# Performance work log

Measured on AMD Instinct MI355X. Metric: run time of the kernel, lower is better.

The kernel has to match this reference:

```python
import jax, jax.numpy as jnp
import numpy as np

VALUE_RANGE = 16
D_MODEL = 1024
NUM_TILES = 8
NUM_FREQS = 6
BATCH = 65536
TEMPERATURE = 0.5


def _fourier(x):
    # x: (B,) -> (B, 2*NUM_FREQS); freqs = 2**[0..F)
    freqs = 2.0 ** jnp.arange(NUM_FREQS, dtype=jnp.float32)
    ang = x[:, None] * (2.0 * np.pi / VALUE_RANGE) * freqs[None, :]
    return jnp.concatenate([jnp.sin(ang), jnp.cos(ang)], axis=-1)


def _layernorm(x, g, b, eps=1e-5):
    m = jnp.mean(x, axis=-1, keepdims=True)
    v = jnp.var(x, axis=-1, keepdims=True)
    return (x - m) * jax.lax.rsqrt(v + eps) * g + b


def _gelu(x):
    return jax.nn.gelu(x, approximate=False)  # torch nn.GELU() default is exact erf


def setup_inputs() -> dict:
    key = jax.random.key(0)
    ks = jax.random.split(key, 16)
    d, T, F4 = D_MODEL, NUM_TILES, 4 * NUM_FREQS
    s = lambda i, shape, scale: (jax.random.normal(ks[i], shape, jnp.float32) * scale)
    return {
        "a": jax.random.uniform(ks[0], (BATCH,), jnp.float32, 0.0, float(VALUE_RANGE)),
        "b": jax.random.uniform(ks[1], (BATCH,), jnp.float32, 0.0, float(VALUE_RANGE)),
        "W_in": s(2, (F4, d), 0.05), "b_in": jnp.zeros((d,), jnp.float32),
        "ln_g": jnp.ones((d,), jnp.float32), "ln_b": jnp.zeros((d,), jnp.float32),
        "Wr1_sum": s(3, (d, d), 0.03), "br1_sum": jnp.zeros((d,), jnp.float32),
        "Wr2_sum": s(4, (d, T), 0.03), "br2_sum": jnp.zeros((T,), jnp.float32),
        "Wr1_diff": s(5, (d, d), 0.03), "br1_diff": jnp.zeros((d,), jnp.float32),
        "Wr2_diff": s(6, (d, T), 0.03), "br2_diff": jnp.zeros((T,), jnp.float32),
        "We1": s(7, (T, d, 2 * d), 0.03), "be1": jnp.zeros((T, 2 * d), jnp.float32),
        "We2": s(8, (T, 2 * d, d), 0.02), "be2": jnp.zeros((T, d), jnp.float32),
        "w_sum": s(9, (d,), 0.03), "bs": jnp.zeros((), jnp.float32),
        "w_diff": s(10, (d,), 0.03), "bd": jnp.zeros((), jnp.float32),
    }


def reference(a, b, W_in, b_in, ln_g, ln_b,
              Wr1_sum, br1_sum, Wr2_sum, br2_sum,
              Wr1_diff, br1_diff, Wr2_diff, br2_diff,
              We1, be1, We2, be2, w_sum, bs, w_diff, bd):
    # Shared encoder
    x = jnp.concatenate([_fourier(a), _fourier(b)], axis=-1)      # (B, 4F)
    x = _gelu(_layernorm(x @ W_in + b_in, ln_g, ln_b))            # (B, d)
    # Top-1 routing (temperature scaling does not change argmax, kept for fidelity)
    sum_logits = (_gelu(x @ Wr1_sum + br1_sum) @ Wr2_sum + br2_sum) / TEMPERATURE
    diff_logits = (_gelu(x @ Wr1_diff + br1_diff) @ Wr2_diff + br2_diff) / TEMPERATURE
    sum_tile = jnp.argmax(sum_logits, axis=-1)                    # (B,)
    diff_tile = jnp.argmax(diff_logits, axis=-1)                  # (B,)
    # Expert dispatch: loop over small fixed num_tiles, mask-combine per token.
    sum_hidden = jnp.zeros_like(x)
    diff_hidden = jnp.zeros_like(x)
    for t in range(We1.shape[0]):
        y = _gelu(x @ We1[t] + be1[t]) @ We2[t] + be2[t]          # (B, d)
        sum_hidden = sum_hidden + jnp.where((sum_tile == t)[:, None], y, 0.0)
        diff_hidden = diff_hidden + jnp.where((diff_tile == t)[:, None], y, 0.0)
    sum_pred = sum_hidden @ w_sum + bs                            # (B,)
    diff_pred = diff_hidden @ w_diff + bd                         # (B,)
    return (sum_pred, diff_pred)
```

## Files before the change

### kernel.cpp

```cpp
#include <hip/hip_runtime.h>
#include <math.h>


#define BT 65536
#define D 1024
#define NT 8
#define DH 2048
#define RCAP 8192
#define DELTA 0.010f
#define XJCAP 768

typedef _Float16 f16;
typedef _Float16 f16x8 __attribute__((ext_vector_type(8)));
typedef _Float16 f16x4 __attribute__((ext_vector_type(4)));
typedef float f32x16 __attribute__((ext_vector_type(16)));

__device__ __forceinline__ float gelu_f(float v) {
    return 0.5f * v * (1.0f + erff(v * 0.70710678118654752440f));
}

__device__ __forceinline__ float gelu_fast(float x) {
    float ax = fabsf(x) * 0.70710678118654752440f;
    float t = __builtin_amdgcn_rcpf(1.0f + 0.3275911f * ax);
    float p = t * (0.254829592f + t * (-0.284496736f + t * (1.421413741f +
              t * (-1.453152027f + t * 1.061405429f))));
    float er = 1.0f - p * __expf(-ax * ax);
    er = copysignf(er, x);
    return 0.5f * x * (1.0f + er);
}

__device__ __forceinline__ void gload16(const void* g, void* l) {
    __builtin_amdgcn_global_load_lds(
        (const __attribute__((address_space(1))) void*)g,
        (__attribute__((address_space(3))) void*)l, 16, 0, 0);
}

__global__ __launch_bounds__(256) void k_prev(
    const float* __restrict__ We2, const float* __restrict__ w_sum,
    const float* __restrict__ w_diff, const float* __restrict__ be2,
    const float* __restrict__ bs, const float* __restrict__ bd,
    float* __restrict__ v_sum, float* __restrict__ v_diff,
    float* __restrict__ c_sum, float* __restrict__ c_diff)
{
    int bid = blockIdx.x;
    if (bid < 4096) {
        int row  = bid * 4 + (threadIdx.x >> 6);
        int lane = threadIdx.x & 63;
        const float* r = We2 + (size_t)row * D;
        float s1 = 0.f, s2 = 0.f;
        #pragma unroll
        for (int i = 0; i < 4; i++) {
            int o4 = (lane + 64 * i) * 4;
            float4 w = *(const float4*)(r + o4);
            float4 u = *(const float4*)(w_sum + o4);
            float4 v = *(const float4*)(w_diff + o4);
            s1 += w.x*u.x + w.y*u.y + w.z*u.z + w.w*u.w;
            s2 += w.x*v.x + w.y*v.y + w.z*v.z + w.w*v.w;
        }
        #pragma unroll
        for (int m = 32; m >= 1; m >>= 1) {
            s1 += __shfl_xor(s1, m, 64);
// ... 36 lines not shown
    for (int i = 0; i < 16; i++) {
        int idx = tid + 256 * i;
        int nn = idx >> 6, kk = idx & 63;
        dst[(size_t)nn * D + kk] = (f16)tile[kk][nn];
    }
}

__global__ __launch_bounds__(256) void k_cvtR(
    const float* __restrict__ Wr1s, const float* __restrict__ Wr1d,
    f16* __restrict__ Wr1Tf)
{
    __shared__ float tile[64][65];
    int b = blockIdx.x;
    int z = b >> 8, rem = b & 255;
    int kt = rem >> 4, nt2 = rem & 15;
    int tid = threadIdx.x;
    const float* W = z ? Wr1d : Wr1s;
    const float* src = W + (size_t)(kt * 64) * 1024 + nt2 * 64;
    #pragma unroll
    for (int i = 0; i < 16; i++) {
        int idx = tid + 256 * i;
        int kk = idx >> 6, nn = idx & 63;
        tile[kk][nn] = src[(size_t)kk * 1024 + nn];
    }
    __syncthreads();
    f16* dst = Wr1Tf + (size_t)(z * 1024 + nt2 * 64) * 1024 + kt * 64;
    #pragma unroll
    for (int i = 0; i < 16; i++) {
        int idx = tid + 256 * i;
        int nn = idx >> 6, kk = idx & 63;
        dst[(size_t)nn * 1024 + kk] = (f16)tile[kk][nn];
    }
}

__global__ __launch_bounds__(256) void k_fuse(
    const float* __restrict__ br1s, const float* __restrict__ br1d,
    const float* __restrict__ Wr2s, const float* __restrict__ Wr2d,
    float* __restrict__ br1f, float* __restrict__ w2f)
{
    int tid = threadIdx.x;
    for (int n = tid; n < 2048; n += 256) {
        br1f[n] = (n < 1024) ? br1s[n] : br1d[n - 1024];
        const float* src = (n < 1024) ? (Wr2s + (size_t)n * 8)
                                      : (Wr2d + (size_t)(n - 1024) * 8);
        #pragma unroll
        for (int o = 0; o < 8; o++) w2f[(size_t)n * 8 + o] = src[o];
    }
}

__global__ __launch_bounds__(256) void k_enc(
    const float* __restrict__ a, const float* __restrict__ b,
    const float* __restrict__ W_in, const float* __restrict__ b_in,
    const float* __restrict__ ln_g, const float* __restrict__ ln_b,
    float* __restrict__ x, f16* __restrict__ xh, int tok0)
{
    __shared__ float x0[64][24];
    __shared__ float red[8];
    int tid = threadIdx.x;
    float4 Wc[24];
    #pragma unroll
    for (int f = 0; f < 24; f++) Wc[f] = *(const float4*)(W_in + f * D + tid * 4);
    float4 bi = *(const float4*)(b_in + tid * 4);
    float4 gg = *(const float4*)(ln_g + tid * 4);
    float4 bb = *(const float4*)(ln_b + tid * 4);
    int base = tok0 + blockIdx.x * 64;

    for (int idx = tid; idx < 64 * 12; idx += 256) {
        int t = idx / 12, q = idx - t * 12;
        int fr = q % 6;
        float in = (q < 6) ? a[base + t] : b[base + t];
        float ang = (in * 0.39269908169872414f) * (float)(1 << fr);
        int off = (q < 6) ? 0 : 12;
        x0[t][off + fr]     = sinf(ang);
        x0[t][off + 6 + fr] = cosf(ang);
    }
    __syncthreads();

    int lane = tid & 63, wid = tid >> 6;
    for (int t = 0; t < 64; t++) {
        float4 p = bi;
        #pragma unroll
        for (int f = 0; f < 24; f++) {
            float xv = x0[t][f];
            p.x += xv * Wc[f].x; p.y += xv * Wc[f].y;
            p.z += xv * Wc[f].z; p.w += xv * Wc[f].w;
        }
        float s1 = p.x + p.y + p.z + p.w;
        float s2 = p.x*p.x + p.y*p.y + p.z*p.z + p.w*p.w;
        #pragma unroll
        for (int m = 32; m >= 1; m >>= 1) {
            s1 += __shfl_xor(s1, m, 64);
            s2 += __shfl_xor(s2, m, 64);
        }
        if (lane == 0) { red[wid] = s1; red[4 + wid] = s2; }
        __syncthreads();
        float mean = (red[0] + red[1] + red[2] + red[3]) * (1.f / 1024.f);
        float ms   = (red[4] + red[5] + red[6] + red[7]) * (1.f / 1024.f);
        float inv  = 1.f / sqrtf(ms - mean * mean + 1e-5f);
        float4 o;
        o.x = gelu_f((p.x - mean) * inv * gg.x + bb.x);
        o.y = gelu_f((p.y - mean) * inv * gg.y + bb.y);
        o.z = gelu_f((p.z - mean) * inv * gg.z + bb.z);
        o.w = gelu_f((p.w - mean) * inv * gg.w + bb.w);
        size_t row = (size_t)(blockIdx.x * 64 + t);
        *(float4*)(x + row * D + tid * 4) = o;
        f16x4 h; h[0] = (f16)o.x; h[1] = (f16)o.y; h[2] = (f16)o.z; h[3] = (f16)o.w;
        *(f16x4*)(xh + row * D + tid * 4) = h;
        __syncthreads();
    }
}

__global__ __launch_bounds__(256, 3) void k_rtrm(
    const f16* __restrict__ xh, const f16* __restrict__ Wr1Tf,
    const float* __restrict__ br1f, const float* __restrict__ w2f,
    float* __restrict__ part)
{
    __shared__ char smem[40960] __attribute__((aligned(16)));
    int bid = blockIdx.x;
    int ntile = bid & 7;
    int ttile = bid >> 3;
    int tid = threadIdx.x;
    int lane = tid & 63, wid = tid >> 6;
    int hi = lane >> 5, l31 = lane & 31;
    int sg = tid >> 3, sc = tid & 7;

    const char* xb = (const char*)xh + (size_t)(ttile * 64) * 2048;
    const char* wb = (const char*)Wr1Tf + (size_t)(ntile * 256) * 2048;
    size_t goff = (size_t)sg * 2048 + (size_t)((sc * 16) ^ ((sg & 7) << 4));

    int axor = (l31 & 7) << 4;
    int kx[4];
    #pragma unroll
    for (int ks = 0; ks < 4; ks++) kx[ks] = (ks * 32 + hi * 16) ^ axor;
    int arow[2], brow[2];
    #pragma unroll
    for (int mi = 0; mi < 2; mi++) arow[mi] = (wid * 64 + mi * 32 + l31) * 128;
    #pragma unroll
    for (int ni = 0; ni < 2; ni++) brow[ni] = 32768 + (ni * 32 + l31) * 128;

    f32x16 acc[2][2];
    #pragma unroll
    for (int mi = 0; mi < 2; mi++)
        #pragma unroll
        for (int ni = 0; ni < 2; ni++) acc[mi][ni] = (f32x16)(0.0f);

    for (int k0 = 0; k0 < 1024; k0 += 64) {
        __syncthreads();
        #pragma unroll
        for (int i = 0; i < 8; i++)
            gload16(wb + (size_t)i * 32 * 2048 + k0 * 2 + goff,
                    smem + i * 4096 + wid * 1024);
        #pragma unroll
        for (int i = 0; i < 2; i++)
            gload16(xb + (size_t)i * 32 * 2048 + k0 * 2 + goff,
                    smem + 32768 + i * 4096 + wid * 1024);
        __syncthreads();
        #pragma unroll
        for (int ks = 0; ks < 4; ks++) {
// ... 4 lines not shown
            acc[0][0] = __builtin_amdgcn_mfma_f32_32x32x16_f16(a0, b0, acc[0][0], 0, 0, 0);
            acc[0][1] = __builtin_amdgcn_mfma_f32_32x32x16_f16(a0, b1, acc[0][1], 0, 0, 0);
            acc[1][0] = __builtin_amdgcn_mfma_f32_32x32x16_f16(a1, b0, acc[1][0], 0, 0, 0);
            acc[1][1] = __builtin_amdgcn_mfma_f32_32x32x16_f16(a1, b1, acc[1][1], 0, 0, 0);
        }
    }

    float lp[2][8] = {};
    #pragma unroll
    for (int mi = 0; mi < 2; mi++) {
        #pragma unroll
        for (int r = 0; r < 16; r++) {
            int nl = wid * 64 + mi * 32 + (r & 3) + 8 * (r >> 2) + 4 * hi;
            int gn = ntile * 256 + nl;
            float b1 = br1f[gn];
            float4 wa = *(const float4*)(w2f + (size_t)gn * 8);
            float4 wc = *(const float4*)(w2f + (size_t)gn * 8 + 4);
            float h0 = gelu_fast(acc[mi][0][r] + b1);
            float h1 = gelu_fast(acc[mi][1][r] + b1);
            lp[0][0] += h0*wa.x; lp[0][1] += h0*wa.y;
            lp[0][2] += h0*wa.z; lp[0][3] += h0*wa.w;
            lp[0][4] += h0*wc.x; lp[0][5] += h0*wc.y;
            lp[0][6] += h0*wc.z; lp[0][7] += h0*wc.w;
            lp[1][0] += h1*wa.x; lp[1][1] += h1*wa.y;
            lp[1][2] += h1*wa.z; lp[1][3] += h1*wa.w;
            lp[1][4] += h1*wc.x; lp[1][5] += h1*wc.y;
            lp[1][6] += h1*wc.z; lp[1][7] += h1*wc.w;
        }
    }
    #pragma unroll
    for (int ni = 0; ni < 2; ni++)
        #pragma unroll
        for (int o = 0; o < 8; o++)
            lp[ni][o] += __shfl_xor(lp[ni][o], 32, 64);
    __syncthreads();
    float* redf = (float*)smem;
    if (hi == 0) {
        #pragma unroll
        for (int ni = 0; ni < 2; ni++)
            #pragma unroll
            for (int o = 0; o < 8; o++)
                redf[(wid * 64 + ni * 32 + l31) * 8 + o] = lp[ni][o];
    }
    __syncthreads();
    for (int idx = tid; idx < 512; idx += 256) {
        int tok = idx >> 3, o = idx & 7;
        float s = ((redf[(0 * 64 + tok) * 8 + o]  + redf[(1 * 64 + tok) * 8 + o])
                 +  redf[(2 * 64 + tok) * 8 + o]) + redf[(3 * 64 + tok) * 8 + o];
        part[((size_t)(ttile * 64 + tok) * 8 + ntile) * 8 + o] = s;
    }
}

__device__ __forceinline__ void emit_tasks(int tok, int ts, int td,
                                           int* tasks, int* cnts, int tstr)
{
    if (ts == td) {
        int s = atomicAdd(&cnts[ts], 1);
        tasks[ts * tstr + s] = tok | (3 << 17);
    } else {
        int s1 = atomicAdd(&cnts[ts], 1);
        tasks[ts * tstr + s1] = tok | (1 << 17);
        int s2 = atomicAdd(&cnts[td], 1);
        tasks[td * tstr + s2] = tok | (2 << 17);
    }
}

__global__ __launch_bounds__(256) void k_amx2(
    const float* __restrict__ part, const float* __restrict__ b2s,
    const float* __restrict__ b2d, int* __restrict__ tasks,
    int* __restrict__ ctrl, int* __restrict__ redoS, int* __restrict__ redoD,
    int tstr)
{
    int i = blockIdx.x * 256 + threadIdx.x;
    const float* p = part + (size_t)i * 64;
    float Ls[8], Ld[8];
    #pragma unroll
    for (int o = 0; o < 8; o++) { Ls[o] = b2s[o]; Ld[o] = b2d[o]; }
    #pragma unroll
    for (int nt = 0; nt < 4; nt++)
        #pragma unroll
        for (int o = 0; o < 8; o++) Ls[o] += p[nt * 8 + o];
    #pragma unroll
    for (int nt = 4; nt < 8; nt++)
        #pragma unroll
        for (int o = 0; o < 8; o++) Ld[o] += p[nt * 8 + o];

    int as = 0; float m1s = Ls[0];
    #pragma unroll
    for (int o = 1; o < 8; o++) if (Ls[o] > m1s) { m1s = Ls[o]; as = o; }
    float m2s = -1e30f;
    #pragma unroll
    for (int o = 0; o < 8; o++) if (o != as && Ls[o] > m2s) m2s = Ls[o];
    int ad = 0; float m1d = Ld[0];
    #pragma unroll
    for (int o = 1; o < 8; o++) if (Ld[o] > m1d) { m1d = Ld[o]; ad = o; }
    float m2d = -1e30f;
    #pragma unroll
    for (int o = 0; o < 8; o++) if (o != ad && Ld[o] > m2d) m2d = Ld[o];

    bool sM = (m1s - m2s) < DELTA;
    bool dM = (m1d - m2d) < DELTA;
    if (!sM && !dM) { emit_tasks(i, as, ad, tasks, ctrl, tstr); return; }
    int posS = -1, posD = -1;
    if (sM) { posS = atomicAdd(&ctrl[8], 1); if (posS >= RCAP) { sM = false; posS = -1; } }
    if (dM) { posD = atomicAdd(&ctrl[9], 1); if (posD >= RCAP) { dM = false; posD = -1; } }
    if (!sM && !dM) { emit_tasks(i, as, ad, tasks, ctrl, tstr); return; }
    if (sM) redoS[posS] = i | (ad << 17) | ((dM ? 1 : 0) << 20);
    if (dM) redoD[posD] = i | (as << 17) | ((sM ? 1 : 0) << 20);
}

__global__ __launch_bounds__(256) void k_redo(
    const float* __restrict__ x,
    const float* __restrict__ Wr1s, const float* __restrict__ br1s,
    const float* __restrict__ Wr2s,
    const float* __restrict__ Wr1d, const float* __restrict__ br1d,
    const float* __restrict__ Wr2d,
    const int* __restrict__ redoS, const int* __restrict__ redoD,
    const int* __restrict__ ctrl,
    float* __restrict__ rlogpS, float* __restrict__ rlogpD)
{
    int nt = blockIdx.y, z = blockIdx.z;
    int rcnt = min(ctrl[8 + z], RCAP);
    const float* Wr1 = z ? Wr1d : Wr1s;
    const float* br1 = z ? br1d : br1s;
    const float* Wr2 = z ? Wr2d : Wr2s;
    const int* list = z ? redoD : redoS;
    float* rlogp = z ? rlogpD : rlogpS;
    __shared__ float As[64][72];
    __shared__ float Bs[64][132];
    __shared__ int tokR[64];
    int tid = threadIdx.x;
    int tr = tid >> 5, tc = tid & 31;

    for (int mc = blockIdx.x; mc * 64 < rcnt; mc += gridDim.x) {
        __syncthreads();
        if (tid < 64) tokR[tid] = list[min(mc * 64 + tid, rcnt - 1)] & 0xFFFF;
        __syncthreads();
        float acc[8][4] = {};
        const float* wb = Wr1 + nt * 128;
        for (int k0 = 0; k0 < D; k0 += 64) {
            __syncthreads();
            {
                int row = tid >> 2, q = tid & 3;
                const float* xr = x + (size_t)tokR[row] * D + k0;
                #pragma unroll
                for (int i = 0; i < 4; i++) {
                    int f4i = q + 4 * i;
                    float4 v = *(const float4*)(xr + f4i * 4);
                    int k = f4i * 4;
                    As[k][row] = v.x; As[k+1][row] = v.y;
                    As[k+2][row] = v.z; As[k+3][row] = v.w;
                }
            }
            {
                #pragma unroll
                for (int i = 0; i < 8; i++) {
                    int idx = tid + 256 * i;
                    int k = idx >> 5, nq = idx & 31;
                    float4 v = *(const float4*)(wb + (size_t)(k0 + k) * D + nq * 4);
                    *(float4*)&Bs[k][nq * 4] = v;
                }
            }
            __syncthreads();
            #pragma unroll 4
            for (int kk = 0; kk < 64; kk++) {
                float4 a0 = *(const float4*)&As[kk][tr * 8];
                float4 a1 = *(const float4*)&As[kk][tr * 8 + 4];
                float4 bv = *(const float4*)&Bs[kk][tc * 4];
                float ar[8] = {a0.x,a0.y,a0.z,a0.w,a1.x,a1.y,a1.z,a1.w};
                #pragma unroll
                for (int i = 0; i < 8; i++) {
                    acc[i][0] += ar[i] * bv.x;
                    acc[i][1] += ar[i] * bv.y;
                    acc[i][2] += ar[i] * bv.z;
                    acc[i][3] += ar[i] * bv.w;
                }
            }
        }
        float lp[8][8] = {};
        #pragma unroll
        for (int j = 0; j < 4; j++) {
            int col = nt * 128 + tc * 4 + j;
            float b1 = br1[col];
            float w2[8];
            #pragma unroll
            for (int o = 0; o < 8; o++) w2[o] = Wr2[col * 8 + o];
            #pragma unroll
            for (int i = 0; i < 8; i++) {
                float h = gelu_f(acc[i][j] + b1);
                #pragma unroll
                for (int o = 0; o < 8; o++) lp[i][o] += h * w2[o];
            }
        }
        #pragma unroll
        for (int m = 16; m >= 1; m >>= 1) {
            #pragma unroll
            for (int i = 0; i < 8; i++)
                #pragma unroll
                for (int o = 0; o < 8; o++)
                    lp[i][o] += __shfl_xor(lp[i][o], m, 64);
        }
        if (tc == 0) {
            #pragma unroll
            for (int i = 0; i < 8; i++) {
                int slot = mc * 64 + tr * 8 + i;
                if (slot < rcnt) {
                    float* p = rlogp + (size_t)slot * 64 + nt * 8;
                    #pragma unroll
                    for (int o = 0; o < 8; o++) p[o] = lp[i][o];
                }
            }
        }
    }
}

__global__ __launch_bounds__(256) void k_amx3d(
    const float* __restrict__ rlogpD, const int* __restrict__ redoD,
    const float* __restrict__ b2d, int* __restrict__ tasks,
    int* __restrict__ ctrl, int* __restrict__ adx, int tstr)
{
    int rcnt = min(ctrl[9], RCAP);
    for (int s = blockIdx.x * 256 + threadIdx.x; s < rcnt; s += gridDim.x * 256) {
        int entry = redoD[s];
        int tok = entry & 0xFFFF;
        float L[8] = {};
        for (int nt = 0; nt < 8; nt++) {
            const float* p = rlogpD + (size_t)s * 64 + nt * 8;
            #pragma unroll
            for (int o = 0; o < 8; o++) L[o] += p[o];
        }
        #pragma unroll
        for (int o = 0; o < 8; o++) L[o] += b2d[o];
        int td = 0; float bv = L[0];
        #pragma unroll
        for (int o = 1; o < 8; o++) if (L[o] > bv) { bv = L[o]; td = o; }
        adx[tok] = td;
        if (!((entry >> 20) & 1))
            emit_tasks(tok, (entry >> 17) & 7, td, tasks, ctrl, tstr);
    }
}

__global__ __launch_bounds__(256) void k_amx3s(
    const float* __restrict__ rlogpS, const int* __restrict__ redoS,
    const float* __restrict__ b2s, int* __restrict__ tasks,
    int* __restrict__ ctrl, const int* __restrict__ adx, int tstr)
{
    int rcnt = min(ctrl[8], RCAP);
    for (int s = blockIdx.x * 256 + threadIdx.x; s < rcnt; s += gridDim.x * 256) {
        int entry = redoS[s];
        int tok = entry & 0xFFFF;
        float L[8] = {};
        for (int nt = 0; nt < 8; nt++) {
            const float* p = rlogpS + (size_t)s * 64 + nt * 8;
            #pragma unroll
            for (int o = 0; o < 8; o++) L[o] += p[o];
        }
        #pragma unroll
        for (int o = 0; o < 8; o++) L[o] += b2s[o];
        int ts = 0; float bv = L[0];
        #pragma unroll
        for (int o = 1; o < 8; o++) if (L[o] > bv) { bv = L[o]; ts = o; }
        int td = ((entry >> 20) & 1) ? adx[tok] : ((entry >> 17) & 7);
        emit_tasks(tok, ts, td, tasks, ctrl, tstr);
    }
}

__global__ void k_sched(const int* __restrict__ ctrl, int* __restrict__ xjob)
{
    __shared__ int seg[17];
    __shared__ int Jt[2];
    int tid = threadIdx.x;
    if (tid == 0) {
        int o = 0;
        for (int e = 0; e < 8; e++) {
            int nt2 = (ctrl[e] + 127) >> 7;
            seg[e * 2]     = o; o += nt2;
            seg[e * 2 + 1] = o; o += nt2;
        }
        seg[16] = o;
        Jt[0] = o; Jt[1] = (o + 7) >> 3;
    }
    __syncthreads();
    int J = Jt[0], target = Jt[1];
    for (int g = tid; g < J; g += blockDim.x) {
        int s = 0;
        while (s < 15 && seg[s + 1] <= g) s++;
        int e = s >> 1, ch = s & 1, rt = g - seg[s];
        int x = g / target; if (x > 7) x = 7;
        int pos = g - x * target;
        xjob[x * XJCAP + pos] = e | (ch << 3) | (rt << 4);
    }
    if (tid < 8) {
        int c = J - tid * target;
        if (c < 0) c = 0;
        if (c > target) c = target;
        xjob[8 * XJCAP + tid] = c;
    }
}

__global__ __launch_bounds__(256) void k_expm(
    const f16* __restrict__ xh, const f16* __restrict__ We1T,
    const float* __restrict__ be1, const float* __restrict__ v_sum,
    const float* __restrict__ v_diff, const float* __restrict__ c_sum,
    const float* __restrict__ c_diff, const int* __restrict__ tasks,
    const int* __restrict__ counts, const int* __restrict__ xjob,
    float* __restrict__ ppS, float* __restrict__ ppD, int qn)
{
    int xcd  = blockIdx.x & 7;
    int slot = blockIdx.x >> 3;
    int nj = xjob[8 * XJCAP + xcd];
    int tstr = 2 * qn;

    __shared__ char smem[49152] __attribute__((aligned(16)));
    __shared__ int tokL[128];
    __shared__ int flgL[128];
    __shared__ float redS[2][128];
    __shared__ float redD[2][128];

    int tid = threadIdx.x;
    int lane = tid & 63;
    int wid  = tid >> 6;
    int wr = wid >> 1, wc = wid & 1;
    int hi = lane >> 5, l31 = lane & 31;
    int sg = tid >> 3, sc = tid & 7;
    int stoff = sg * 128 + ((sc * 16) ^ ((sg & 7) << 4));

    const char* xh_b = (const char*)xh;

    int axor = (l31 & 7) << 4;
    int kx[4];
    #pragma unroll
    for (int ks = 0; ks < 4; ks++) kx[ks] = (ks * 32 + hi * 16) ^ axor;
    int arow[2], nrow[4];
    #pragma unroll
    for (int mi = 0; mi < 2; mi++) arow[mi] = (wr * 64 + mi * 32 + l31) * 128;
    #pragma unroll
    for (int ni = 0; ni < 4; ni++) nrow[ni] = 16384 + (wc * 128 + ni * 32 + l31) * 128;

    for (int j = slot; j < nj; j += 256) {
        int jv = xjob[xcd * XJCAP + j];
        int e  = jv & 7;
        int ch = (jv >> 3) & 1;
        int rt = jv >> 4;
        int cnt = counts[e];
        int r0 = rt * 128;
        const char* we1t_e = (const char*)(We1T + (size_t)e * DH * D);
        size_t bs_off = (size_t)sg * (D * 2) + sc * 16;

        __syncthreads();
        if (tid < 128) {
            int idx = r0 + tid;
            int tv = tasks[e * tstr + min(idx, cnt - 1)];
            tokL[tid] = tv & 0xFFFF;
            flgL[tid] = (idx < cnt) ? ((tv >> 17) & 3) : 0;
        }
        __syncthreads();
        size_t asrc_off[4];
        #pragma unroll
        for (int i = 0; i < 4; i++)
            asrc_off[i] = (size_t)tokL[i * 32 + sg] * (D * 2) + sc * 16;

        float ss[2][16] = {}, sd[2][16] = {};

        for (int n0 = ch * 1024; n0 < ch * 1024 + 1024; n0 += 256) {
            f32x16 acc[2][4];
            #pragma unroll
            for (int mi = 0; mi < 2; mi++)
                #pragma unroll
                for (int ni = 0; ni < 4; ni++)
                    acc[mi][ni] = (f32x16)(0.0f);

            const char* bsrc0 = we1t_e + (size_t)n0 * (D * 2) + bs_off;

            for (int k0 = 0; k0 < D; k0 += 64) {
                __syncthreads();
                #pragma unroll
                for (int i = 0; i < 4; i++) {
                    int4 v = *(const int4*)(xh_b + asrc_off[i] + k0 * 2);
                    *(int4*)(smem + i * 4096 + stoff) = v;
                }
                #pragma unroll
                for (int i = 0; i < 8; i++) {
                    int4 v = *(const int4*)(bsrc0 + (size_t)i * 32 * (D * 2) + k0 * 2);
                    *(int4*)(smem + 16384 + i * 4096 + stoff) = v;
                }
                __syncthreads();
                #pragma unroll
                for (int ks = 0; ks < 4; ks++) {
                    f16x8 a0 = *(const f16x8*)(smem + arow[0] + kx[ks]);
                    f16x8 a1 = *(const f16x8*)(smem + arow[1] + kx[ks]);
                    #pragma unroll
                    for (int ni = 0; ni < 4; ni++) {
                        f16x8 bf = *(const f16x8*)(smem + nrow[ni] + kx[ks]);
                        acc[0][ni] = __builtin_amdgcn_mfma_f32_32x32x16_f16(a0, bf, acc[0][ni], 0, 0, 0);
                        acc[1][ni] = __builtin_amdgcn_mfma_f32_32x32x16_f16(a1, bf, acc[1][ni], 0, 0, 0);
                    }
                }
            }
            #pragma unroll
            for (int ni = 0; ni < 4; ni++) {
                int col = n0 + wc * 128 + ni * 32 + l31;
                float b1 = be1[e * DH + col];
                float vs = v_sum[(size_t)e * DH + col];
                float vd = v_diff[(size_t)e * DH + col];
                #pragma unroll
                for (int mi = 0; mi < 2; mi++) {
                    #pragma unroll
                    for (int r = 0; r < 16; r++) {
                        float h = gelu_fast(acc[mi][ni][r] + b1);
                        ss[mi][r] += h * vs;
                        sd[mi][r] += h * vd;
                    }
                }
            }
        }

        #pragma unroll
        for (int m = 16; m >= 1; m >>= 1) {
            #pragma unroll
            for (int mi = 0; mi < 2; mi++)
                #pragma unroll
                for (int r = 0; r < 16; r++) {
                    ss[mi][r] += __shfl_xor(ss[mi][r], m, 64);
                    sd[mi][r] += __shfl_xor(sd[mi][r], m, 64);
                }
        }
        if (l31 == 0) {
            #pragma unroll
            for (int mi = 0; mi < 2; mi++)
                #pragma unroll
                for (int r = 0; r < 16; r++) {
                    int row = wr * 64 + mi * 32 + (r & 3) + 8 * (r >> 2) + 4 * hi;
                    redS[wc][row] = ss[mi][r];
                    redD[wc][row] = sd[mi][r];
                }
        }
        __syncthreads();
        if (tid < 128) {
            int idx = r0 + tid;
            if (idx < cnt) {
                int fl = flgL[tid];
                int tok = tokL[tid];
                float s = redS[0][tid] + redS[1][tid];
                float d = redD[0][tid] + redD[1][tid];
                if (ch == 0) { s += c_sum[e]; d += c_diff[e]; }
                if (fl & 1) ppS[ch * qn + tok] = s;
                if (fl & 2) ppD[ch * qn + tok] = d;
            }
        }
    }
}

__global__ __launch_bounds__(256) void k_fin(
    const float* __restrict__ ppS, const float* __restrict__ ppD,
    float* __restrict__ out, int tok0, int qn)
{
    int i = blockIdx.x * 256 + threadIdx.x;
    out[tok0 + i]      = ppS[i] + ppS[qn + i];
    out[BT + tok0 + i] = ppD[i] + ppD[qn + i];
}

extern "C" void kernel_launch(void* const* d_in, const int* in_sizes, int n_in,
                              void* d_out, int out_size, void* d_ws, size_t ws_size,
                              hipStream_t stream)
{
    const float* a      = (const float*)d_in[0];
    const float* b      = (const float*)d_in[1];
    const float* W_in   = (const float*)d_in[2];
    const float* b_in   = (const float*)d_in[3];
    const float* ln_g   = (const float*)d_in[4];
    const float* ln_b   = (const float*)d_in[5];
    const float* Wr1s   = (const float*)d_in[6];
    const float* br1s   = (const float*)d_in[7];
    const float* Wr2s   = (const float*)d_in[8];
    const float* br2s   = (const float*)d_in[9];
    const float* Wr1d   = (const float*)d_in[10];
    const float* br1d   = (const float*)d_in[11];
    const float* Wr2d   = (const float*)d_in[12];
    const float* br2d   = (const float*)d_in[13];
    const float* We1    = (const float*)d_in[14];
    const float* be1    = (const float*)d_in[15];
    const float* We2    = (const float*)d_in[16];
    const float* be2    = (const float*)d_in[17];
    const float* w_sum  = (const float*)d_in[18];
    const float* bs     = (const float*)d_in[19];
    const float* w_diff = (const float*)d_in[20];
    const float* bd     = (const float*)d_in[21];
    float* out = (float*)d_out;

    auto plan = [&](size_t qn) -> size_t {
        size_t o = 0;
        auto al = [&](size_t bytes) { o = (o + bytes + 255) & ~(size_t)255; };
        al((size_t)NT * DH * 4); al((size_t)NT * DH * 4); al(64); al(64);
        al(qn * D * 4); al(qn * D * 2); al(qn * 64 * 4);
        al((size_t)RCAP * 64 * 4); al((size_t)RCAP * 64 * 4);
        al((size_t)RCAP * 4); al((size_t)RCAP * 4); al(qn * 4);
        al((size_t)NT * 2 * qn * 4);
        al(64); al((size_t)(8 * XJCAP + 8) * 4);
        al(2 * qn * 4); al(2 * qn * 4);
        al((size_t)NT * DH * D * 2); al((size_t)2048 * 1024 * 2);
        al(2048 * 4); al(2048 * 8 * 4);
        return o;
    };
    int qn = 65536;
    while (qn > 16384 && plan((size_t)qn) > ws_size) qn >>= 1;
    if (plan((size_t)qn) > ws_size) {
        hipMemsetAsync(d_out, 0, (size_t)out_size * 4, stream);
        return;
    }
    int npass = BT / qn;
    int tstr = 2 * qn;

    char* w = (char*)d_ws;
    size_t off = 0;
    auto alloc = [&](size_t bytes) -> char* {
        char* p = w + off;
        off = (off + bytes + 255) & ~(size_t)255;
        return p;
    };
    float* v_sum   = (float*)alloc((size_t)NT * DH * 4);
    float* v_diff  = (float*)alloc((size_t)NT * DH * 4);
    float* c_sum   = (float*)alloc(64);
    float* c_diff  = (float*)alloc(64);
    float* x       = (float*)alloc((size_t)qn * D * 4);
    f16*   xh      = (f16*)alloc((size_t)qn * D * 2);
    float* part    = (float*)alloc((size_t)qn * 64 * 4);
    float* rlogpS  = (float*)alloc((size_t)RCAP * 64 * 4);
    float* rlogpD  = (float*)alloc((size_t)RCAP * 64 * 4);
    int*   redoS   = (int*)alloc((size_t)RCAP * 4);
    int*   redoD   = (int*)alloc((size_t)RCAP * 4);
    int*   adx     = (int*)alloc((size_t)qn * 4);
    int*   tasks   = (int*)alloc((size_t)NT * 2 * qn * 4);
    int*   ctrl    = (int*)alloc(64);
    int*   xjob    = (int*)alloc((size_t)(8 * XJCAP + 8) * 4);
    float* ppS     = (float*)alloc((size_t)2 * qn * 4);
    float* ppD     = (float*)alloc((size_t)2 * qn * 4);
    f16*   We1T    = (f16*)alloc((size_t)NT * DH * D * 2);
    f16*   Wr1Tf   = (f16*)alloc((size_t)2048 * 1024 * 2);
    float* br1f    = (float*)alloc((size_t)2048 * 4);
    float* w2f     = (float*)alloc((size_t)2048 * 8 * 4);

    k_cvt <<<dim3(4096), dim3(256), 0, stream>>>(We1, We1T);
    k_cvtR<<<dim3(512),  dim3(256), 0, stream>>>(Wr1s, Wr1d, Wr1Tf);
    k_fuse<<<dim3(1),    dim3(256), 0, stream>>>(br1s, br1d, Wr2s, Wr2d, br1f, w2f);
    k_prev<<<dim3(4097), dim3(256), 0, stream>>>(We2, w_sum, w_diff, be2, bs, bd,
                                                 v_sum, v_diff, c_sum, c_diff);
    for (int q = 0; q < npass; q++) {
        int tok0 = q * qn;
        k_enc<<<dim3(qn / 64), dim3(256), 0, stream>>>(a, b, W_in, b_in, ln_g, ln_b, x, xh, tok0);
        k_rtrm<<<dim3(qn / 64 * 8), dim3(256), 0, stream>>>(xh, Wr1Tf, br1f, w2f, part);
        hipMemsetAsync(ctrl, 0, 64, stream);
        k_amx2<<<dim3(qn / 256), dim3(256), 0, stream>>>(part, br2s, br2d, tasks, ctrl,
                                                         redoS, redoD, tstr);
        k_redo<<<dim3(32, 8, 2), dim3(256), 0, stream>>>(x, Wr1s, br1s, Wr2s, Wr1d, br1d, Wr2d,
                                                         redoS, redoD, ctrl, rlogpS, rlogpD);
        k_amx3d<<<dim3(16), dim3(256), 0, stream>>>(rlogpD, redoD, br2d, tasks, ctrl, adx, tstr);
        k_amx3s<<<dim3(16), dim3(256), 0, stream>>>(rlogpS, redoS, br2s, tasks, ctrl, adx, tstr);
        k_sched<<<dim3(1), dim3(256), 0, stream>>>(ctrl, xjob);
        k_expm<<<dim3(2048), dim3(256), 0, stream>>>(xh, We1T, be1, v_sum, v_diff,
                                                     c_sum, c_diff, tasks, ctrl, xjob,
                                                     ppS, ppD, qn);
        k_fin<<<dim3(qn / 256), dim3(256), 0, stream>>>(ppS, ppD, out, tok0, qn);
    }
}
```

Baseline: 2.474 ms.

## Drop fp32 activation buffer, recompute encoder in redo, restructure expert GEMM loop

The encoder no longer writes a 256MB fp32 copy of the activations. The redo kernel now recomputes the encoder for each ambiguous token in small groups and computes the full router row per block, instead of tiling over a stored fp32 buffer. The expert GEMM kernel flattens its N/K loops into a single loop with register-prefetched B tiles and sets launch bounds to 2 blocks per SM. The multi-pass planning is removed, so buffers are sized for a single full-batch pass and the task stride is halved. This saves encoder write bandwidth at the cost of some redundant encoder compute and a fixed workspace requirement.

```diff
diff --git a/kernel.cpp b/kernel.cpp
--- a/kernel.cpp
+++ b/kernel.cpp
@@ -3,10 +3,13 @@
 
 
 #define BT 65536
+#define QN 65536
+#define TSTR QN
 #define D 1024
 #define NT 8
 #define DH 2048
 #define RCAP 8192
+#define RTOK 8
 #define DELTA 0.010f
 #define XJCAP 768
 
@@ -149,7 +152,7 @@
     const float* __restrict__ a, const float* __restrict__ b,
     const float* __restrict__ W_in, const float* __restrict__ b_in,
     const float* __restrict__ ln_g, const float* __restrict__ ln_b,
-    float* __restrict__ x, f16* __restrict__ xh, int tok0)
+    f16* __restrict__ xh)
 {
     __shared__ float x0[64][24];
     __shared__ float red[8];
@@ -160,7 +163,7 @@
     float4 bi = *(const float4*)(b_in + tid * 4);
     float4 gg = *(const float4*)(ln_g + tid * 4);
     float4 bb = *(const float4*)(ln_b + tid * 4);
-    int base = tok0 + blockIdx.x * 64;
+    int base = blockIdx.x * 64;
 
     for (int idx = tid; idx < 64 * 12; idx += 256) {
         int t = idx / 12, q = idx - t * 12;
@@ -200,7 +203,6 @@
         o.z = gelu_f((p.z - mean) * inv * gg.z + bb.z);
         o.w = gelu_f((p.w - mean) * inv * gg.w + bb.w);
         size_t row = (size_t)(blockIdx.x * 64 + t);
-        *(float4*)(x + row * D + tid * 4) = o;
         f16x4 h; h[0] = (f16)o.x; h[1] = (f16)o.y; h[2] = (f16)o.z; h[3] = (f16)o.w;
         *(f16x4*)(xh + row * D + tid * 4) = h;
         __syncthreads();
@@ -311,24 +313,23 @@
 }
 
 __device__ __forceinline__ void emit_tasks(int tok, int ts, int td,
-                                           int* tasks, int* cnts, int tstr)
+                                           int* tasks, int* cnts)
 {
     if (ts == td) {
         int s = atomicAdd(&cnts[ts], 1);
-        tasks[ts * tstr + s] = tok | (3 << 17);
+        tasks[ts * TSTR + s] = tok | (3 << 17);
     } else {
         int s1 = atomicAdd(&cnts[ts], 1);
-        tasks[ts * tstr + s1] = tok | (1 << 17);
+        tasks[ts * TSTR + s1] = tok | (1 << 17);
         int s2 = atomicAdd(&cnts[td], 1);
-        tasks[td * tstr + s2] = tok | (2 << 17);
+        tasks[td * TSTR + s2] = tok | (2 << 17);
     }
 }
 
 __global__ __launch_bounds__(256) void k_amx2(
     const float* __restrict__ part, const float* __restrict__ b2s,
     const float* __restrict__ b2d, int* __restrict__ tasks,
-    int* __restrict__ ctrl, int* __restrict__ redoS, int* __restrict__ redoD,
-    int tstr)
+    int* __restrict__ ctrl, int* __restrict__ redoS, int* __restrict__ redoD)
 {
     int i = blockIdx.x * 256 + threadIdx.x;
     const float* p = part + (size_t)i * 64;
@@ -359,17 +360,19 @@
 
     bool sM = (m1s - m2s) < DELTA;
     bool dM = (m1d - m2d) < DELTA;
-    if (!sM && !dM) { emit_tasks(i, as, ad, tasks, ctrl, tstr); return; }
+    if (!sM && !dM) { emit_tasks(i, as, ad, tasks, ctrl); return; }
     int posS = -1, posD = -1;
     if (sM) { posS = atomicAdd(&ctrl[8], 1); if (posS >= RCAP) { sM = false; posS = -1; } }
     if (dM) { posD = atomicAdd(&ctrl[9], 1); if (posD >= RCAP) { dM = false; posD = -1; } }
-    if (!sM && !dM) { emit_tasks(i, as, ad, tasks, ctrl, tstr); return; }
+    if (!sM && !dM) { emit_tasks(i, as, ad, tasks, ctrl); return; }
     if (sM) redoS[posS] = i | (ad << 17) | ((dM ? 1 : 0) << 20);
     if (dM) redoD[posD] = i | (as << 17) | ((sM ? 1 : 0) << 20);
 }
 
 __global__ __launch_bounds__(256) void k_redo(
-    const float* __restrict__ x,
+    const float* __restrict__ a, const float* __restrict__ b,
+    const float* __restrict__ W_in, const float* __restrict__ b_in,
+    const float* __restrict__ ln_g, const float* __restrict__ ln_b,
     const float* __restrict__ Wr1s, const float* __restrict__ br1s,
     const float* __restrict__ Wr2s,
     const float* __restrict__ Wr1d, const float* __restrict__ br1d,
@@ -378,97 +381,128 @@
     const int* __restrict__ ctrl,
     float* __restrict__ rlogpS, float* __restrict__ rlogpD)
 {
-    int nt = blockIdx.y, z = blockIdx.z;
+    int z = blockIdx.y;
     int rcnt = min(ctrl[8 + z], RCAP);
+    int s0 = blockIdx.x * RTOK;
+    if (s0 >= rcnt) return;
+    const int* list = z ? redoD : redoS;
     const float* Wr1 = z ? Wr1d : Wr1s;
-    const float* br1 = z ? br1d : br1s;
+    const float* br1v = z ? br1d : br1s;
     const float* Wr2 = z ? Wr2d : Wr2s;
-    const int* list = z ? redoD : redoS;
-    float* rlogp = z ? rlogpD : rlogpS;
-    __shared__ float As[64][72];
-    __shared__ float Bs[64][132];
-    __shared__ int tokR[64];
+
+    __shared__ float xl[RTOK][1024];
+    __shared__ float x0[RTOK][24];
+    __shared__ float wred[4][RTOK][2];
+    __shared__ float lred[4][RTOK][8];
+    __shared__ int tokR[RTOK];
     int tid = threadIdx.x;
-    int tr = tid >> 5, tc = tid & 31;
-
-    for (int mc = blockIdx.x; mc * 64 < rcnt; mc += gridDim.x) {
+    int lane = tid & 63, wid = tid >> 6;
+
+    if (tid < RTOK) tokR[tid] = list[min(s0 + tid, rcnt - 1)] & 0xFFFF;
+    __syncthreads();
+
+    if (tid < RTOK * 12) {
+        int t = tid / 12, q = tid - t * 12;
+        int fr = q % 6;
+        int tok = tokR[t];
+        float in = (q < 6) ? a[tok] : b[tok];
+        float ang = (in * 0.39269908169872414f) * (float)(1 << fr);
+        int off = (q < 6) ? 0 : 12;
+        x0[t][off + fr]     = sinf(ang);
+        x0[t][off + 6 + fr] = cosf(ang);
+    }
+    __syncthreads();
+
+    {
+        float4 Wc[24];
+        #pragma unroll
+        for (int f = 0; f < 24; f++) Wc[f] = *(const float4*)(W_in + f * D + tid * 4);
+        float4 bi = *(const float4*)(b_in + tid * 4);
+        float4 gg = *(const float4*)(ln_g + tid * 4);
+        float4 bb = *(const float4*)(ln_b + tid * 4);
+        float p[RTOK][4];
+        #pragma unroll
+        for (int r = 0; r < RTOK; r++) {
+            float4 pv = bi;
+            #pragma unroll
+            for (int f = 0; f < 24; f++) {
+                float xv = x0[r][f];
+                pv.x += xv * Wc[f].x; pv.y += xv * Wc[f].y;
+                pv.z += xv * Wc[f].z; pv.w += xv * Wc[f].w;
+            }
+            p[r][0] = pv.x; p[r][1] = pv.y; p[r][2] = pv.z; p[r][3] = pv.w;
+            float s1 = pv.x + pv.y + pv.z + pv.w;
+            float s2 = pv.x*pv.x + pv.y*pv.y + pv.z*pv.z + pv.w*pv.w;
+            #pragma unroll
+            for (int m = 32; m >= 1; m >>= 1) {
+                s1 += __shfl_xor(s1, m, 64);
+                s2 += __shfl_xor(s2, m, 64);
+            }
+            if (lane == 0) { wred[wid][r][0] = s1; wred[wid][r][1] = s2; }
+        }
         __syncthreads();
-        if (tid < 64) tokR[tid] = list[min(mc * 64 + tid, rcnt - 1)] & 0xFFFF;
-        __syncthreads();
-        float acc[8][4] = {};
-        const float* wb = Wr1 + nt * 128;
-        for (int k0 = 0; k0 < D; k0 += 64) {
-            __syncthreads();
-            {
-                int row = tid >> 2, q = tid & 3;
-                const float* xr = x + (size_t)tokR[row] * D + k0;
-                #pragma unroll
-                for (int i = 0; i < 4; i++) {
-                    int f4i = q + 4 * i;
-                    float4 v = *(const float4*)(xr + f4i * 4);
-                    int k = f4i * 4;
-                    As[k][row] = v.x; As[k+1][row] = v.y;
-                    As[k+2][row] = v.z; As[k+3][row] = v.w;
-                }
-            }
-            {
-                #pragma unroll
-                for (int i = 0; i < 8; i++) {
-                    int idx = tid + 256 * i;
-                    int k = idx >> 5, nq = idx & 31;
-                    float4 v = *(const float4*)(wb + (size_t)(k0 + k) * D + nq * 4);
-                    *(float4*)&Bs[k][nq * 4] = v;
-                }
-            }
-            __syncthreads();
-            #pragma unroll 4
-            for (int kk = 0; kk < 64; kk++) {
-                float4 a0 = *(const float4*)&As[kk][tr * 8];
-                float4 a1 = *(const float4*)&As[kk][tr * 8 + 4];
-                float4 bv = *(const float4*)&Bs[kk][tc * 4];
-                float ar[8] = {a0.x,a0.y,a0.z,a0.w,a1.x,a1.y,a1.z,a1.w};
-                #pragma unroll
-                for (int i = 0; i < 8; i++) {
-                    acc[i][0] += ar[i] * bv.x;
-                    acc[i][1] += ar[i] * bv.y;
-                    acc[i][2] += ar[i] * bv.z;
-                    acc[i][3] += ar[i] * bv.w;
-                }
-            }
-        }
-        float lp[8][8] = {};
-        #pragma unroll
-        for (int j = 0; j < 4; j++) {
-            int col = nt * 128 + tc * 4 + j;
-            float b1 = br1[col];
-            float w2[8];
-            #pragma unroll
-            for (int o = 0; o < 8; o++) w2[o] = Wr2[col * 8 + o];
-            #pragma unroll
-            for (int i = 0; i < 8; i++) {
-                float h = gelu_f(acc[i][j] + b1);
-                #pragma unroll
-                for (int o = 0; o < 8; o++) lp[i][o] += h * w2[o];
-            }
-        }
-        #pragma unroll
-        for (int m = 16; m >= 1; m >>= 1) {
-            #pragma unroll
-            for (int i = 0; i < 8; i++)
-                #pragma unroll
-                for (int o = 0; o < 8; o++)
-                    lp[i][o] += __shfl_xor(lp[i][o], m, 64);
-        }
-        if (tc == 0) {
-            #pragma unroll
-            for (int i = 0; i < 8; i++) {
-                int slot = mc * 64 + tr * 8 + i;
-                if (slot < rcnt) {
-                    float* p = rlogp + (size_t)slot * 64 + nt * 8;
-                    #pragma unroll
-                    for (int o = 0; o < 8; o++) p[o] = lp[i][o];
-                }
-            }
+        #pragma unroll
+        for (int r = 0; r < RTOK; r++) {
+            float mean = (wred[0][r][0] + wred[1][r][0] + wred[2][r][0] + wred[3][r][0]) * (1.f / 1024.f);
+            float ms   = (wred[0][r][1] + wred[1][r][1] + wred[2][r][1] + wred[3][r][1]) * (1.f / 1024.f);
+            float inv  = 1.f / sqrtf(ms - mean * mean + 1e-5f);
+            float gv[4] = {gg.x, gg.y, gg.z, gg.w};
+            float bv[4] = {bb.x, bb.y, bb.z, bb.w};
+            #pragma unroll
+            for (int jj = 0; jj < 4; jj++)
+                xl[r][tid * 4 + jj] = gelu_f((p[r][jj] - mean) * inv * gv[jj] + bv[jj]);
+        }
+    }
+    __syncthreads();
+
+    int c0 = tid * 4;
+    float hacc[RTOK][4] = {};
+    #pragma unroll 4
+    for (int k = 0; k < 1024; k++) {
+        float4 wv = *(const float4*)(Wr1 + (size_t)k * 1024 + c0);
+        #pragma unroll
+        for (int r = 0; r < RTOK; r++) {
+            float xv = xl[r][k];
+            hacc[r][0] += xv * wv.x; hacc[r][1] += xv * wv.y;
+            hacc[r][2] += xv * wv.z; hacc[r][3] += xv * wv.w;
+        }
+    }
+    float L[RTOK][8] = {};
+    #pragma unroll
+    for (int jj = 0; jj < 4; jj++) {
+        int col = c0 + jj;
+        float b1 = br1v[col];
+        float4 wa = *(const float4*)(Wr2 + (size_t)col * 8);
+        float4 wc = *(const float4*)(Wr2 + (size_t)col * 8 + 4);
+        #pragma unroll
+        for (int r = 0; r < RTOK; r++) {
+            float h = gelu_f(hacc[r][jj] + b1);
+            L[r][0] += h*wa.x; L[r][1] += h*wa.y; L[r][2] += h*wa.z; L[r][3] += h*wa.w;
+            L[r][4] += h*wc.x; L[r][5] += h*wc.y; L[r][6] += h*wc.z; L[r][7] += h*wc.w;
+        }
+    }
+    #pragma unroll
+    for (int m = 32; m >= 1; m >>= 1)
+        #pragma unroll
+        for (int r = 0; r < RTOK; r++)
+            #pragma unroll
+            for (int o = 0; o < 8; o++)
+                L[r][o] += __shfl_xor(L[r][o], m, 64);
+    if (lane == 0) {
+        #pragma unroll
+        for (int r = 0; r < RTOK; r++)
+            #pragma unroll
+            for (int o = 0; o < 8; o++)
+                lred[wid][r][o] = L[r][o];
+    }
+    __syncthreads();
+    if (tid < RTOK * 8) {
+        int r = tid >> 3, o = tid & 7;
+        int slot = s0 + r;
+        if (slot < rcnt) {
+            float v = ((lred[0][r][o] + lred[1][r][o]) + lred[2][r][o]) + lred[3][r][o];
+            float* dst = z ? rlogpD : rlogpS;
+            dst[(size_t)slot * 8 + o] = v;
         }
     }
 }
@@ -476,51 +510,41 @@
 __global__ __launch_bounds__(256) void k_amx3d(
     const float* __restrict__ rlogpD, const int* __restrict__ redoD,
     const float* __restrict__ b2d, int* __restrict__ tasks,
-    int* __restrict__ ctrl, int* __restrict__ adx, int tstr)
+    int* __restrict__ ctrl, int* __restrict__ adx)
 {
     int rcnt = min(ctrl[9], RCAP);
     for (int s = blockIdx.x * 256 + threadIdx.x; s < rcnt; s += gridDim.x * 256) {
         int entry = redoD[s];
         int tok = entry & 0xFFFF;
-        float L[8] = {};
-        for (int nt = 0; nt < 8; nt++) {
-            const float* p = rlogpD + (size_t)s * 64 + nt * 8;
-            #pragma unroll
-            for (int o = 0; o < 8; o++) L[o] += p[o];
-        }
-        #pragma unroll
-        for (int o = 0; o < 8; o++) L[o] += b2d[o];
+        float L[8];
+        #pragma unroll
+        for (int o = 0; o < 8; o++) L[o] = rlogpD[(size_t)s * 8 + o] + b2d[o];
         int td = 0; float bv = L[0];
         #pragma unroll
         for (int o = 1; o < 8; o++) if (L[o] > bv) { bv = L[o]; td = o; }
         adx[tok] = td;
         if (!((entry >> 20) & 1))
-            emit_tasks(tok, (entry >> 17) & 7, td, tasks, ctrl, tstr);
+            emit_tasks(tok, (entry >> 17) & 7, td, tasks, ctrl);
     }
 }
 
 __global__ __launch_bounds__(256) void k_amx3s(
     const float* __restrict__ rlogpS, const int* __restrict__ redoS,
     const float* __restrict__ b2s, int* __restrict__ tasks,
-    int* __restrict__ ctrl, const int* __restrict__ adx, int tstr)
+    int* __restrict__ ctrl, const int* __restrict__ adx)
 {
     int rcnt = min(ctrl[8], RCAP);
     for (int s = blockIdx.x * 256 + threadIdx.x; s < rcnt; s += gridDim.x * 256) {
         int entry = redoS[s];
         int tok = entry & 0xFFFF;
-        float L[8] = {};
-        for (int nt = 0; nt < 8; nt++) {
-            const float* p = rlogpS + (size_t)s * 64 + nt * 8;
-            #pragma unroll
-            for (int o = 0; o < 8; o++) L[o] += p[o];
-        }
-        #pragma unroll
-        for (int o = 0; o < 8; o++) L[o] += b2s[o];
+        float L[8];
+        #pragma unroll
+        for (int o = 0; o < 8; o++) L[o] = rlogpS[(size_t)s * 8 + o] + b2s[o];
         int ts = 0; float bv = L[0];
         #pragma unroll
         for (int o = 1; o < 8; o++) if (L[o] > bv) { bv = L[o]; ts = o; }
         int td = ((entry >> 20) & 1) ? adx[tok] : ((entry >> 17) & 7);
-        emit_tasks(tok, ts, td, tasks, ctrl, tstr);
+        emit_tasks(tok, ts, td, tasks, ctrl);
     }
 }
 
@@ -557,18 +581,17 @@
     }
 }
 
-__global__ __launch_bounds__(256) void k_expm(
+__global__ __launch_bounds__(256, 2) void k_expm(
     const f16* __restrict__ xh, const f16* __restrict__ We1T,
     const float* __restrict__ be1, const float* __restrict__ v_sum,
     const float* __restrict__ v_diff, const float* __restrict__ c_sum,
     const float* __restrict__ c_diff, const int* __restrict__ tasks,
     const int* __restrict__ counts, const int* __restrict__ xjob,
-    float* __restrict__ ppS, float* __restrict__ ppD, int qn)
+    float* __restrict__ ppS, float* __restrict__ ppD)
 {
     int xcd  = blockIdx.x & 7;
     int slot = blockIdx.x >> 3;
     int nj = xjob[8 * XJCAP + xcd];
-    int tstr = 2 * qn;
 
     __shared__ char smem[49152] __attribute__((aligned(16)));
     __shared__ int tokL[128];
@@ -603,74 +626,91 @@
         int rt = jv >> 4;
         int cnt = counts[e];
         int r0 = rt * 128;
-        const char* we1t_e = (const char*)(We1T + (size_t)e * DH * D);
-        size_t bs_off = (size_t)sg * (D * 2) + sc * 16;
+        const char* bbase = (const char*)(We1T + (size_t)e * DH * D) + sg * 2048 + sc * 16;
 
         __syncthreads();
         if (tid < 128) {
             int idx = r0 + tid;
-            int tv = tasks[e * tstr + min(idx, cnt - 1)];
+            int tv = tasks[e * TSTR + min(idx, cnt - 1)];
             tokL[tid] = tv & 0xFFFF;
             flgL[tid] = (idx < cnt) ? ((tv >> 17) & 3) : 0;
         }
         __syncthreads();
-        size_t asrc_off[4];
+        int asrc[4];
         #pragma unroll
         for (int i = 0; i < 4; i++)
-            asrc_off[i] = (size_t)tokL[i * 32 + sg] * (D * 2) + sc * 16;
+            asrc[i] = tokL[i * 32 + sg] * 2048 + sc * 16;
 
         float ss[2][16] = {}, sd[2][16] = {};
-
-        for (int n0 = ch * 1024; n0 < ch * 1024 + 1024; n0 += 256) {
-            f32x16 acc[2][4];
-            #pragma unroll
-            for (int mi = 0; mi < 2; mi++)
+        f32x16 acc[2][4];
+        #pragma unroll
+        for (int mi = 0; mi < 2; mi++)
+            #pragma unroll
+            for (int ni = 0; ni < 4; ni++) acc[mi][ni] = (f32x16)(0.0f);
+
+        int nbase = ch * 1024 * 2048;
+
+        int4 rB[8];
+        #pragma unroll
+        for (int i = 0; i < 8; i++)
+            rB[i] = *(const int4*)(bbase + nbase + i * 32 * 2048);
+
+        for (int it = 0; it < 64; ++it) {
+            int k0 = (it & 15) * 64;
+            __syncthreads();
+            {
+                int4 rA[4];
                 #pragma unroll
-                for (int ni = 0; ni < 4; ni++)
-                    acc[mi][ni] = (f32x16)(0.0f);
-
-            const char* bsrc0 = we1t_e + (size_t)n0 * (D * 2) + bs_off;
-
-            for (int k0 = 0; k0 < D; k0 += 64) {
-                __syncthreads();
+                for (int i = 0; i < 4; i++)
+                    rA[i] = *(const int4*)(xh_b + asrc[i] + k0 * 2);
                 #pragma unroll
-                for (int i = 0; i < 4; i++) {
-                    int4 v = *(const int4*)(xh_b + asrc_off[i] + k0 * 2);
-                    *(int4*)(smem + i * 4096 + stoff) = v;
+                for (int i = 0; i < 4; i++)
+                    *(int4*)(smem + i * 4096 + stoff) = rA[i];
+            }
+            #pragma unroll
+            for (int i = 0; i < 8; i++)
+                *(int4*)(smem + 16384 + i * 4096 + stoff) = rB[i];
+            __syncthreads();
+            if (it < 63) {
+                int nit = it + 1;
+                int noff = nbase + ((nit >> 4) * 256) * 2048 + (nit & 15) * 128;
+                #pragma unroll
+                for (int i = 0; i < 8; i++)
+                    rB[i] = *(const int4*)(bbase + noff + i * 32 * 2048);
+            }
+            #pragma unroll
+            for (int ks = 0; ks < 4; ks++) {
+                f16x8 a0 = *(const f16x8*)(smem + arow[0] + kx[ks]);
+                f16x8 a1 = *(const f16x8*)(smem + arow[1] + kx[ks]);
+                #pragma unroll
+                for (int ni = 0; ni < 4; ni++) {
+                    f16x8 bf = *(const f16x8*)(smem + nrow[ni] + kx[ks]);
+                    acc[0][ni] = __builtin_amdgcn_mfma_f32_32x32x16_f16(a0, bf, acc[0][ni], 0, 0, 0);
+                    acc[1][ni] = __builtin_amdgcn_mfma_f32_32x32x16_f16(a1, bf, acc[1][ni], 0, 0, 0);
+                }
+            }
+            if ((it & 15) == 15) {
+                int n0 = ch * 1024 + (it >> 4) * 256;
+                #pragma unroll
+                for (int ni = 0; ni < 4; ni++) {
+                    int col = n0 + wc * 128 + ni * 32 + l31;
+                    float b1 = be1[e * DH + col];
+                    float vs = v_sum[(size_t)e * DH + col];
+                    float vd = v_diff[(size_t)e * DH + col];
+                    #pragma unroll
+                    for (int mi = 0; mi < 2; mi++) {
+                        #pragma unroll
+                        for (int r = 0; r < 16; r++) {
+                            float h = gelu_fast(acc[mi][ni][r] + b1);
+                            ss[mi][r] += h * vs;
+                            sd[mi][r] += h * vd;
+                        }
+                    }
                 }
                 #pragma unroll
-                for (int i = 0; i < 8; i++) {
-                    int4 v = *(const int4*)(bsrc0 + (size_t)i * 32 * (D * 2) + k0 * 2);
-                    *(int4*)(smem + 16384 + i * 4096 + stoff) = v;
-                }
-                __syncthreads();
-                #pragma unroll
-                for (int ks = 0; ks < 4; ks++) {
-                    f16x8 a0 = *(const f16x8*)(smem + arow[0] + kx[ks]);
-                    f16x8 a1 = *(const f16x8*)(smem + arow[1] + kx[ks]);
+                for (int mi = 0; mi < 2; mi++)
                     #pragma unroll
-                    for (int ni = 0; ni < 4; ni++) {
-                        f16x8 bf = *(const f16x8*)(smem + nrow[ni] + kx[ks]);
-                        acc[0][ni] = __builtin_amdgcn_mfma_f32_32x32x16_f16(a0, bf, acc[0][ni], 0, 0, 0);
-                        acc[1][ni] = __builtin_amdgcn_mfma_f32_32x32x16_f16(a1, bf, acc[1][ni], 0, 0, 0);
-                    }
-                }
-            }
-            #pragma unroll
-            for (int ni = 0; ni < 4; ni++) {
-                int col = n0 + wc * 128 + ni * 32 + l31;
-                float b1 = be1[e * DH + col];
-                float vs = v_sum[(size_t)e * DH + col];
-                float vd = v_diff[(size_t)e * DH + col];
-                #pragma unroll
-                for (int mi = 0; mi < 2; mi++) {
-                    #pragma unroll
-                    for (int r = 0; r < 16; r++) {
-                        float h = gelu_fast(acc[mi][ni][r] + b1);
-                        ss[mi][r] += h * vs;
-                        sd[mi][r] += h * vd;
-                    }
-                }
+                    for (int ni = 0; ni < 4; ni++) acc[mi][ni] = (f32x16)(0.0f);
             }
         }
 
@@ -703,8 +743,8 @@
                 float s = redS[0][tid] + redS[1][tid];
                 float d = redD[0][tid] + redD[1][tid];
                 if (ch == 0) { s += c_sum[e]; d += c_diff[e]; }
-                if (fl & 1) ppS[ch * qn + tok] = s;
-                if (fl & 2) ppD[ch * qn + tok] = d;
+                if (fl & 1) ppS[ch * QN + tok] = s;
+                if (fl & 2) ppD[ch * QN + tok] = d;
             }
         }
     }
@@ -712,11 +752,11 @@
 
 __global__ __launch_bounds__(256) void k_fin(
     const float* __restrict__ ppS, const float* __restrict__ ppD,
-    float* __restrict__ out, int tok0, int qn)
+    float* __restrict__ out)
 {
     int i = blockIdx.x * 256 + threadIdx.x;
-    out[tok0 + i]      = ppS[i] + ppS[qn + i];
-    out[BT + tok0 + i] = ppD[i] + ppD[qn + i];
+    out[i]      = ppS[i] + ppS[QN + i];
+    out[BT + i] = ppD[i] + ppD[QN + i];
 }
 
 extern "C" void kernel_launch(void* const* d_in, const int* in_sizes, int n_in,
@@ -747,29 +787,6 @@
     const float* bd     = (const float*)d_in[21];
     float* out = (float*)d_out;
 
-    auto plan = [&](size_t qn) -> size_t {
-        size_t o = 0;
-        auto al = [&](size_t bytes) { o = (o + bytes + 255) & ~(size_t)255; };
-        al((size_t)NT * DH * 4); al((size_t)NT * DH * 4); al(64); al(64);
-        al(qn * D * 4); al(qn * D * 2); al(qn * 64 * 4);
-        al((size_t)RCAP * 64 * 4); al((size_t)RCAP * 64 * 4);
-        al((size_t)RCAP * 4); al((size_t)RCAP * 4); al(qn * 4);
-        al((size_t)NT * 2 * qn * 4);
-        al(64); al((size_t)(8 * XJCAP + 8) * 4);
-        al(2 * qn * 4); al(2 * qn * 4);
-        al((size_t)NT * DH * D * 2); al((size_t)2048 * 1024 * 2);
-        al(2048 * 4); al(2048 * 8 * 4);
-        return o;
-    };
-    int qn = 65536;
-    while (qn > 16384 && plan((size_t)qn) > ws_size) qn >>= 1;
-    if (plan((size_t)qn) > ws_size) {
-        hipMemsetAsync(d_out, 0, (size_t)out_size * 4, stream);
-        return;
-    }
-    int npass = BT / qn;
-    int tstr = 2 * qn;
-
     char* w = (char*)d_ws;
     size_t off = 0;
     auto alloc = [&](size_t bytes) -> char* {
@@ -781,44 +798,46 @@
     float* v_diff  = (float*)alloc((size_t)NT * DH * 4);
     float* c_sum   = (float*)alloc(64);
     float* c_diff  = (float*)alloc(64);
-    float* x       = (float*)alloc((size_t)qn * D * 4);
-    f16*   xh      = (f16*)alloc((size_t)qn * D * 2);
-    float* part    = (float*)alloc((size_t)qn * 64 * 4);
-    float* rlogpS  = (float*)alloc((size_t)RCAP * 64 * 4);
-    float* rlogpD  = (float*)alloc((size_t)RCAP * 64 * 4);
+    f16*   xh      = (f16*)alloc((size_t)QN * D * 2);
+    float* part    = (float*)alloc((size_t)QN * 64 * 4);
+    float* rlogpS  = (float*)alloc((size_t)RCAP * 8 * 4);
+    float* rlogpD  = (float*)alloc((size_t)RCAP * 8 * 4);
     int*   redoS   = (int*)alloc((size_t)RCAP * 4);
     int*   redoD   = (int*)alloc((size_t)RCAP * 4);
-    int*   adx     = (int*)alloc((size_t)qn * 4);
-    int*   tasks   = (int*)alloc((size_t)NT * 2 * qn * 4);
+    int*   adx     = (int*)alloc((size_t)QN * 4);
+    int*   tasks   = (int*)alloc((size_t)NT * QN * 4);
     int*   ctrl    = (int*)alloc(64);
     int*   xjob    = (int*)alloc((size_t)(8 * XJCAP + 8) * 4);
-    float* ppS     = (float*)alloc((size_t)2 * qn * 4);
-    float* ppD     = (float*)alloc((size_t)2 * qn * 4);
+    float* ppS     = (float*)alloc((size_t)2 * QN * 4);
+    float* ppD     = (float*)alloc((size_t)2 * QN * 4);
     f16*   We1T    = (f16*)alloc((size_t)NT * DH * D * 2);
     f16*   Wr1Tf   = (f16*)alloc((size_t)2048 * 1024 * 2);
     float* br1f    = (float*)alloc((size_t)2048 * 4);
     float* w2f     = (float*)alloc((size_t)2048 * 8 * 4);
+    if (off > ws_size) {
+        hipMemsetAsync(d_out, 0, (size_t)out_size * 4, stream);
+        return;
+    }
 
     k_cvt <<<dim3(4096), dim3(256), 0, stream>>>(We1, We1T);
     k_cvtR<<<dim3(512),  dim3(256), 0, stream>>>(Wr1s, Wr1d, Wr1Tf);
     k_fuse<<<dim3(1),    dim3(256), 0, stream>>>(br1s, br1d, Wr2s, Wr2d, br1f, w2f);
     k_prev<<<dim3(4097), dim3(256), 0, stream>>>(We2, w_sum, w_diff, be2, bs, bd,
                                                  v_sum, v_diff, c_sum, c_diff);
-    for (int q = 0; q < npass; q++) {
-        int tok0 = q * qn;
-        k_enc<<<dim3(qn / 64), dim3(256), 0, stream>>>(a, b, W_in, b_in, ln_g, ln_b, x, xh, tok0);
-        k_rtrm<<<dim3(qn / 64 * 8), dim3(256), 0, stream>>>(xh, Wr1Tf, br1f, w2f, part);
-        hipMemsetAsync(ctrl, 0, 64, stream);
-        k_amx2<<<dim3(qn / 256), dim3(256), 0, stream>>>(part, br2s, br2d, tasks, ctrl,
-                                                         redoS, redoD, tstr);
-        k_redo<<<dim3(32, 8, 2), dim3(256), 0, stream>>>(x, Wr1s, br1s, Wr2s, Wr1d, br1d, Wr2d,
-                                                         redoS, redoD, ctrl, rlogpS, rlogpD);
-        k_amx3d<<<dim3(16), dim3(256), 0, stream>>>(rlogpD, redoD, br2d, tasks, ctrl, adx, tstr);
-        k_amx3s<<<dim3(16), dim3(256), 0, stream>>>(rlogpS, redoS, br2s, tasks, ctrl, adx, tstr);
-        k_sched<<<dim3(1), dim3(256), 0, stream>>>(ctrl, xjob);
-        k_expm<<<dim3(2048), dim3(256), 0, stream>>>(xh, We1T, be1, v_sum, v_diff,
-                                                     c_sum, c_diff, tasks, ctrl, xjob,
-                                                     ppS, ppD, qn);
-        k_fin<<<dim3(qn / 256), dim3(256), 0, stream>>>(ppS, ppD, out, tok0, qn);
-    }
-}
+    k_enc<<<dim3(QN / 64), dim3(256), 0, stream>>>(a, b, W_in, b_in, ln_g, ln_b, xh);
+    k_rtrm<<<dim3(QN / 64 * 8), dim3(256), 0, stream>>>(xh, Wr1Tf, br1f, w2f, part);
+    hipMemsetAsync(ctrl, 0, 64, stream);
+    k_amx2<<<dim3(QN / 256), dim3(256), 0, stream>>>(part, br2s, br2d, tasks, ctrl,
+                                                     redoS, redoD);
+    k_redo<<<dim3(RCAP / RTOK, 2), dim3(256), 0, stream>>>(
+        a, b, W_in, b_in, ln_g, ln_b,
+        Wr1s, br1s, Wr2s, Wr1d, br1d, Wr2d,
+        redoS, redoD, ctrl, rlogpS, rlogpD);
+    k_amx3d<<<dim3(16), dim3(256), 0, stream>>>(rlogpD, redoD, br2d, tasks, ctrl, adx);
+    k_amx3s<<<dim3(16), dim3(256), 0, stream>>>(rlogpS, redoS, br2s, tasks, ctrl, adx);
+    k_sched<<<dim3(1), dim3(256), 0, stream>>>(ctrl, xjob);
+    k_expm<<<dim3(2048), dim3(256), 0, stream>>>(xh, We1T, be1, v_sum, v_diff,
+                                                 c_sum, c_diff, tasks, ctrl, xjob,
+                                                 ppS, ppD);
+    k_fin<<<dim3(QN / 256), dim3(256), 0, stream>>>(ppS, ppD, out);
+}
```

After: 3.569 ms. 1.44x slower.
